# Kernel optimization log

Measured on AMD Instinct MI355X. Metric: run time of the kernel, lower is better.

The kernel has to match this reference:

```python
import jax, jax.numpy as jnp
import numpy as np

K = 8
W_CONST = 0.01
EPS = 1e-8


def _normalize(v, eps=1e-8):
    return v / (jnp.linalg.norm(v, axis=-1, keepdims=True) + eps)


def _coarse_normal(x, vertices, vertex_normals):
    # x: (N,3); vertices, vertex_normals: (V,3)
    # brute-force KNN (ascending by squared distance, like cKDTree.query)
    d2_all = jnp.sum((x[:, None, :] - vertices[None, :, :]) ** 2, axis=-1)  # (N,V)
    neg_d2, idx = jax.lax.top_k(-d2_all, K)  # sorted ascending distance
    d2 = -neg_d2                                                    # (N,K)
    v_knn = vertices[idx]                                           # (N,K,3)
    n_knn = vertex_normals[idx]                                     # (N,K,3)
    d2c = jnp.maximum(d2, EPS)
    inv_d2 = 1.0 / d2c                                              # (N,K)
    term_knn = jnp.sum(n_knn * inv_d2[..., None], axis=1)           # (N,3)
    v1 = v_knn[:, 0]                                                # nearest vertex
    d2_v1 = jnp.maximum(jnp.sum((x - v1) ** 2, axis=-1), EPS)       # (N,)
    term_dir = (x - v1) / (W_CONST * d2_v1[:, None])
    W = jnp.sum(inv_d2, axis=1) + 1.0 / W_CONST                     # (N,)
    n_tilde = (term_knn + term_dir) / W[:, None]
    nc = _normalize(n_tilde)
    return nc, v1


def _ray_mesh_first_hit(origins, dirs, tri0, e1, e2):
    # Moller-Trumbore, all points vs all faces. origins/dirs: (N,3); tri0/e1/e2: (F,3)
    pvec = jnp.cross(dirs[:, None, :], e2[None, :, :])              # (N,F,3)
    det = jnp.einsum('fk,nfk->nf', e1, pvec)                        # (N,F)
    ok_det = jnp.abs(det) > EPS
    inv_det = jnp.where(ok_det, 1.0 / jnp.where(ok_det, det, 1.0), 0.0)
    tvec = origins[:, None, :] - tri0[None, :, :]                   # (N,F,3)
    u = jnp.sum(tvec * pvec, axis=-1) * inv_det
    qvec = jnp.cross(tvec, e1[None, :, :])                          # (N,F,3)
    v = jnp.einsum('nk,nfk->nf', dirs, qvec) * inv_det
    t = jnp.einsum('fk,nfk->nf', e2, qvec) * inv_det
    valid = ok_det & (u >= 0.0) & (v >= 0.0) & (u + v <= 1.0) & (t > EPS)
    t_masked = jnp.where(valid, t, jnp.inf)
    t_min = jnp.min(t_masked, axis=1)                               # first hit along ray
    hit = jnp.isfinite(t_min)
    loc = origins + dirs * jnp.where(hit, t_min, 0.0)[:, None]
    return hit, loc


def _project(x, vertices, vertex_normals, faces):
    nc, v1 = _coarse_normal(x, vertices, vertex_normals)
    tri0 = vertices[faces[:, 0]]
    e1 = vertices[faces[:, 1]] - tri0
    e2 = vertices[faces[:, 2]] - tri0
    # primary cast along -nc
    hit1, loc1 = _ray_mesh_first_hit(x, -nc, tri0, e1, e2)
    # fallback cast toward nearest vertex
    dir_fb = _normalize(v1 - x)
    hit2, loc2 = _ray_mesh_first_hit(x, dir_fb, tri0, e1, e2)
    xc = jnp.where(hit1[:, None], loc1, jnp.where(hit2[:, None], loc2, v1))
    s = jnp.sum((x - xc) * nc, axis=-1, keepdims=True)              # (N,1)
    return xc, s, nc


def setup_inputs() -> dict:
    key = jax.random.key(0)
    k1, k2, k3, k4 = jax.random.split(key, 4)
    N, V, F = 2048, 8192, 8192
    x = jax.random.normal(k1, (N, 3), dtype=jnp.float32)
    vertices = jax.random.normal(k2, (V, 3), dtype=jnp.float32)
    vertex_normals = _normalize(jax.random.normal(k3, (V, 3), dtype=jnp.float32))
    faces = jax.random.randint(k4, (F, 3), 0, V, dtype=jnp.int32)
    return {"x": x, "vertices": vertices, "vertex_normals": vertex_normals, "faces": faces}


def reference(x, vertices, vertex_normals, faces):
    # returns (xc:(N,3), s:(N,1), nc:(N,3)) like ProjectionFn.forward
    return _project(x, vertices, vertex_normals, faces)
```

## Files before the change

### kernel.cpp

```cpp
#include <hip/hip_runtime.h>
#include <math.h>

#pragma float_control(precise, on)

#define EPSF 1e-8f


__global__ void __launch_bounds__(512) knn_prep_kernel(
    const float* __restrict__ x, const float* __restrict__ verts,
    const float* __restrict__ vnorm, const int* __restrict__ faces,
    float* __restrict__ tri, float* __restrict__ ncw,
    float* __restrict__ v1w, float* __restrict__ dfbw,
    int N, int V, int F) {
#pragma clang fp contract(off)
    int b = blockIdx.x;
    int tid = threadIdx.x;
    int wave = tid >> 6;
    int lane = tid & 63;
    int pA = 2 * b;
    if (pA >= N) return;
    int pB = pA + 1;
    bool hasB = pB < N;
    int pBs = hasB ? pB : pA;

    for (int gt = b * 512 + tid; gt < F; gt += gridDim.x * 512) {
        int f0 = faces[gt * 3 + 0];
        int f1 = faces[gt * 3 + 1];
        int f2 = faces[gt * 3 + 2];
        float t0x = verts[f0 * 3 + 0], t0y = verts[f0 * 3 + 1], t0z = verts[f0 * 3 + 2];
        float ax = verts[f1 * 3 + 0], ay = verts[f1 * 3 + 1], az = verts[f1 * 3 + 2];
        float bx = verts[f2 * 3 + 0], by = verts[f2 * 3 + 1], bz = verts[f2 * 3 + 2];
        float4* t4 = (float4*)(tri + (size_t)gt * 12);
        t4[0] = make_float4(t0x, t0y, t0z, ax - t0x);
        t4[1] = make_float4(ay - t0y, az - t0z, bx - t0x, by - t0y);
        t4[2] = make_float4(bz - t0z, 0.f, 0.f, 0.f);
    }

    float axx = x[pA * 3 + 0], axy = x[pA * 3 + 1], axz = x[pA * 3 + 2];
    float bxx = x[pBs * 3 + 0], bxy = x[pBs * 3 + 1], bxz = x[pBs * 3 + 2];

    unsigned long long la[8], lb[8];
#pragma unroll
    for (int i = 0; i < 8; ++i) { la[i] = ~0ULL; lb[i] = ~0ULL; }

    for (int v = tid; v < V; v += 512) {
        float vx = verts[v * 3 + 0];
        float vy = verts[v * 3 + 1];
        float vz = verts[v * 3 + 2];

        float dxa = axx - vx, dya = axy - vy, dza = axz - vz;
        float d2a = ((dxa * dxa) + (dya * dya)) + (dza * dza);
        unsigned long long kA =
            (((unsigned long long)__float_as_uint(d2a)) << 32) | (unsigned int)v;
        if (kA < la[7]) {
            la[7] = kA;
#pragma unroll
            for (int j = 7; j > 0; --j) {
                if (la[j] < la[j - 1]) {
                    unsigned long long t = la[j];
                    la[j] = la[j - 1];
                    la[j - 1] = t;
                }
            }
        }

        float dxb = bxx - vx, dyb = bxy - vy, dzb = bxz - vz;
        float d2b = ((dxb * dxb) + (dyb * dyb)) + (dzb * dzb);
        unsigned long long kB =
            (((unsigned long long)__float_as_uint(d2b)) << 32) | (unsigned int)v;
        if (kB < lb[7]) {
            lb[7] = kB;
#pragma unroll
            for (int j = 7; j > 0; --j) {
                if (lb[j] < lb[j - 1]) {
                    unsigned long long t = lb[j];
                    lb[j] = lb[j - 1];
                    lb[j - 1] = t;
                }
            }
        }
    }

    __shared__ unsigned long long candA[64], candB[64];
#pragma unroll
    for (int j = 0; j < 8; ++j) {
        unsigned long long mA = la[0];
        unsigned long long mB = lb[0];
#pragma unroll
        for (int s = 1; s < 64; s <<= 1) {
            unsigned long long oA = __shfl_xor(mA, s, 64);
            if (oA < mA) mA = oA;
            unsigned long long oB = __shfl_xor(mB, s, 64);
            if (oB < mB) mB = oB;
        }
        if (la[0] == mA) {
#pragma unroll
            for (int t = 0; t < 7; ++t) la[t] = la[t + 1];
            la[7] = ~0ULL;
        }
        if (lb[0] == mB) {
#pragma unroll
            for (int t = 0; t < 7; ++t) lb[t] = lb[t + 1];
            lb[7] = ~0ULL;
        }
        if (lane == 0) { candA[wave * 8 + j] = mA; candB[wave * 8 + j] = mB; }
    }
    __syncthreads();

    if (wave > 1) return;
    if (wave == 1 && !hasB) return;

    unsigned long long c0 = (wave == 0) ? candA[lane] : candB[lane];
    unsigned long long sel[8];
#pragma unroll
    for (int j = 0; j < 8; ++j) {
        unsigned long long m = c0;
#pragma unroll
        for (int s = 1; s < 64; s <<= 1) {
            unsigned long long o = __shfl_xor(m, s, 64);
            if (o < m) m = o;
        }
        if (c0 == m) c0 = ~0ULL;
        sel[j] = m;
    }

    if (lane != 0) return;
    int p = (wave == 0) ? pA : pB;
    float xx = (wave == 0) ? axx : bxx;
    float xy = (wave == 0) ? axy : bxy;
    float xz = (wave == 0) ? axz : bxz;

    float invk[8];
    float nsx = 0.f, nsy = 0.f, nsz = 0.f;
#pragma unroll
    for (int j = 0; j < 8; ++j) {
        int id = (int)(sel[j] & 0xffffffffu);
        float d2 = __uint_as_float((unsigned int)(sel[j] >> 32));
        float inv = 1.0f / fmaxf(d2, EPSF);
        invk[j] = inv;
        nsx = nsx + vnorm[id * 3 + 0] * inv;
        nsy = nsy + vnorm[id * 3 + 1] * inv;
        nsz = nsz + vnorm[id * 3 + 2] * inv;
    }
    float Wsum = ((invk[0] + invk[1]) + (invk[2] + invk[3])) +
                 ((invk[4] + invk[5]) + (invk[6] + invk[7]));

    int id0 = (int)(sel[0] & 0xffffffffu);
    float v1x = verts[id0 * 3 + 0];
    float v1y = verts[id0 * 3 + 1];
    float v1z = verts[id0 * 3 + 2];

    float dxv = xx - v1x, dyv = xy - v1y, dzv = xz - v1z;
    float d2v1 = fmaxf(((dxv * dxv) + (dyv * dyv)) + (dzv * dzv), EPSF);
    float den = 0.01f * d2v1;
    float tdx = dxv / den, tdy = dyv / den, tdz = dzv / den;

    float W = Wsum + 100.0f;
    float ntx = (nsx + tdx) / W;
    float nty = (nsy + tdy) / W;
    float ntz = (nsz + tdz) / W;
    float nrm = sqrtf(((ntx * ntx) + (nty * nty)) + (ntz * ntz)) + 1e-8f;
    float ncx = ntx / nrm, ncy = nty / nrm, ncz = ntz / nrm;

    float fx = v1x - xx, fy = v1y - xy, fz = v1z - xz;
    float fn = sqrtf(((fx * fx) + (fy * fy)) + (fz * fz)) + 1e-8f;
    fx = fx / fn; fy = fy / fn; fz = fz / fn;

    ncw[p * 3 + 0] = ncx; ncw[p * 3 + 1] = ncy; ncw[p * 3 + 2] = ncz;
    v1w[p * 3 + 0] = v1x; v1w[p * 3 + 1] = v1y; v1w[p * 3 + 2] = v1z;
    dfbw[p * 3 + 0] = fx; dfbw[p * 3 + 1] = fy; dfbw[p * 3 + 2] = fz;
}

__device__ __forceinline__ float mt_test(
    float ox, float oy, float oz, float dx, float dy, float dz,
    const float4 A, const float4 B, const float4 C, float tb) {
#pragma clang fp contract(off)
    const float M = 1e-5f;
    float e1x = A.w, e1y = B.x, e1z = B.y;
    float e2x = B.z, e2y = B.w, e2z = C.x;
    float tvx = ox - A.x;
    float tvy = oy - A.y;
    float tvz = oz - A.z;
    float qx = (tvy * e1z) - (tvz * e1y);
    float qy = (tvz * e1x) - (tvx * e1z);
    float qz = (tvx * e1y) - (tvy * e1x);
    float tq = ((e2x * qx) + (e2y * qy)) + (e2z * qz);
    float px = (dy * e2z) - (dz * e2y);
    float py = (dz * e2x) - (dx * e2z);
    float pz = (dx * e2y) - (dy * e2x);
    float det = ((e1x * px) + (e1y * py)) + (e1z * pz);
    bool ok = fabsf(det) > EPSF;
    float inv = ok ? (1.0f / det) : 0.0f;
    float u = (((tvx * px) + (tvy * py)) + (tvz * pz)) * inv;
    float v = (((dx * qx) + (dy * qy)) + (dz * qz)) * inv;
    float t = tq * inv;
    bool valid = ok && (u >= -M) && (v >= -M) && ((u + v) <= 1.0f + M) && (t > EPSF);
    return (valid && t < tb) ? t : tb;
}

__global__ void __launch_bounds__(512) ray_fin_kernel(
    const float* __restrict__ x, const float* __restrict__ tri,
    const float* __restrict__ ncw, const float* __restrict__ v1w,
    const float* __restrict__ dfbw, float* __restrict__ out, int N, int F) {
#pragma clang fp contract(off)
    __shared__ unsigned int redA[8], redB[8];
    __shared__ unsigned int u1As, u1Bs, u2As, u2Bs, hAf, hBf;
    int b = blockIdx.x;
    int tid = threadIdx.x;
    int wave = tid >> 6;
    int lane = tid & 63;
    int pA = 2 * b;
    if (pA >= N) return;
    int pB = pA + 1;
    bool hasB = pB < N;
    int pBs = hasB ? pB : pA;

    float axx = x[pA * 3 + 0], axy = x[pA * 3 + 1], axz = x[pA * 3 + 2];
    float Ancx = ncw[pA * 3 + 0], Ancy = ncw[pA * 3 + 1], Ancz = ncw[pA * 3 + 2];
    float Adbx = dfbw[pA * 3 + 0], Adby = dfbw[pA * 3 + 1], Adbz = dfbw[pA * 3 + 2];
    float Adax = -Ancx, Aday = -Ancy, Adaz = -Ancz;

    float bxx = x[pBs * 3 + 0], bxy = x[pBs * 3 + 1], bxz = x[pBs * 3 + 2];
    float Bncx = ncw[pBs * 3 + 0], Bncy = ncw[pBs * 3 + 1], Bncz = ncw[pBs * 3 + 2];
    float Bdbx = dfbw[pBs * 3 + 0], Bdby = dfbw[pBs * 3 + 1], Bdbz = dfbw[pBs * 3 + 2];
    float Bdax = -Bncx, Bday = -Bncy, Bdaz = -Bncz;

    const float INF = __uint_as_float(0x7f800000u);

    float tA = INF, tB = INF;
    for (int fi = tid; fi < F; fi += 512) {
        const float4 A4 = *(const float4*)(tri + (size_t)fi * 12);
        const float4 B4 = *(const float4*)(tri + (size_t)fi * 12 + 4);
        const float4 C4 = *(const float4*)(tri + (size_t)fi * 12 + 8);
        tA = mt_test(axx, axy, axz, Adax, Aday, Adaz, A4, B4, C4, tA);
        tB = mt_test(bxx, bxy, bxz, Bdax, Bday, Bdaz, A4, B4, C4, tB);
    }

    {
        unsigned int ma = __float_as_uint(tA);
        unsigned int mb = __float_as_uint(tB);
#pragma unroll
        for (int s = 1; s < 64; s <<= 1) {
            unsigned int oa = __shfl_xor(ma, s, 64);
            if (oa < ma) ma = oa;
            unsigned int ob = __shfl_xor(mb, s, 64);
            if (ob < mb) mb = ob;
        }
        if (lane == 0) { redA[wave] = ma; redB[wave] = mb; }
    }
    __syncthreads();
    if (tid == 0) {
        unsigned int u1A = min(min(min(redA[0], redA[1]), min(redA[2], redA[3])),
                               min(min(redA[4], redA[5]), min(redA[6], redA[7])));
        unsigned int u1B = min(min(min(redB[0], redB[1]), min(redB[2], redB[3])),
                               min(min(redB[4], redB[5]), min(redB[6], redB[7])));
        u1As = u1A; u1Bs = u1B;
        hAf = (u1A < 0x7f800000u) ? 1u : 0u;
        hBf = (u1B < 0x7f800000u) ? 1u : 0u;
    }
    __syncthreads();

    bool needA = (hAf == 0u);
    bool needB = hasB && (hBf == 0u);
    if (needA || needB) {
        float sA = INF, sB = INF;
        for (int fi = tid; fi < F; fi += 512) {
            const float4 A4 = *(const float4*)(tri + (size_t)fi * 12);
            const float4 B4 = *(const float4*)(tri + (size_t)fi * 12 + 4);
            const float4 C4 = *(const float4*)(tri + (size_t)fi * 12 + 8);
            if (needA) sA = mt_test(axx, axy, axz, Adbx, Adby, Adbz, A4, B4, C4, sA);
            if (needB) sB = mt_test(bxx, bxy, bxz, Bdbx, Bdby, Bdbz, A4, B4, C4, sB);
        }
        unsigned int ma = __float_as_uint(sA);
        unsigned int mb = __float_as_uint(sB);
#pragma unroll
        for (int s = 1; s < 64; s <<= 1) {
            unsigned int oa = __shfl_xor(ma, s, 64);
            if (oa < ma) ma = oa;
            unsigned int ob = __shfl_xor(mb, s, 64);
            if (ob < mb) mb = ob;
        }
        if (lane == 0) { redA[wave] = ma; redB[wave] = mb; }
        __syncthreads();
        if (tid == 0) {
            u2As = min(min(min(redA[0], redA[1]), min(redA[2], redA[3])),
                       min(min(redA[4], redA[5]), min(redA[6], redA[7])));
            u2Bs = min(min(min(redB[0], redB[1]), min(redB[2], redB[3])),
                       min(min(redB[4], redB[5]), min(redB[6], redB[7])));
        }
    }

    if (tid != 0) return;
    {
        float t1 = __uint_as_float(u1As);
        bool h1 = t1 < INF;
        float t2 = h1 ? INF : __uint_as_float(u2As);
        bool h2 = t2 < INF;
        float xcx, xcy, xcz;
        if (h1) {
            xcx = axx + ((-Ancx) * t1);
            xcy = axy + ((-Ancy) * t1);
            xcz = axz + ((-Ancz) * t1);
        } else if (h2) {
            xcx = axx + (Adbx * t2);
            xcy = axy + (Adby * t2);
            xcz = axz + (Adbz * t2);
        } else {
            xcx = v1w[pA * 3 + 0]; xcy = v1w[pA * 3 + 1]; xcz = v1w[pA * 3 + 2];
        }
        float s = (((axx - xcx) * Ancx) + ((axy - xcy) * Ancy)) + ((axz - xcz) * Ancz);
        out[pA * 3 + 0] = xcx;
        out[pA * 3 + 1] = xcy;
        out[pA * 3 + 2] = xcz;
        out[3 * N + pA] = s;
        out[4 * N + pA * 3 + 0] = Ancx;
        out[4 * N + pA * 3 + 1] = Ancy;
        out[4 * N + pA * 3 + 2] = Ancz;
    }
    if (hasB) {
        float t1 = __uint_as_float(u1Bs);
        bool h1 = t1 < INF;
        float t2 = h1 ? INF : __uint_as_float(u2Bs);
        bool h2 = t2 < INF;
        float xcx, xcy, xcz;
        if (h1) {
            xcx = bxx + ((-Bncx) * t1);
            xcy = bxy + ((-Bncy) * t1);
            xcz = bxz + ((-Bncz) * t1);
        } else if (h2) {
            xcx = bxx + (Bdbx * t2);
            xcy = bxy + (Bdby * t2);
            xcz = bxz + (Bdbz * t2);
        } else {
            xcx = v1w[pB * 3 + 0]; xcy = v1w[pB * 3 + 1]; xcz = v1w[pB * 3 + 2];
        }
        float s = (((bxx - xcx) * Bncx) + ((bxy - xcy) * Bncy)) + ((bxz - xcz) * Bncz);
        out[pB * 3 + 0] = xcx;
        out[pB * 3 + 1] = xcy;
        out[pB * 3 + 2] = xcz;
        out[3 * N + pB] = s;
        out[4 * N + pB * 3 + 0] = Bncx;
        out[4 * N + pB * 3 + 1] = Bncy;
        out[4 * N + pB * 3 + 2] = Bncz;
    }
}

extern "C" void kernel_launch(void* const* d_in, const int* in_sizes, int n_in,
                              void* d_out, int out_size, void* d_ws, size_t ws_size,
                              hipStream_t stream) {
    const float* x     = (const float*)d_in[0];
    const float* verts = (const float*)d_in[1];
    const float* vnorm = (const float*)d_in[2];
    const int*   faces = (const int*)d_in[3];
    int N = in_sizes[0] / 3;
    int V = in_sizes[1] / 3;
    int F = in_sizes[3] / 3;

    float* tri  = (float*)d_ws;
    float* ncw  = tri + (size_t)F * 12;
    float* v1w  = ncw + 3 * N;
    float* dfbw = v1w + 3 * N;

    int pblocks = (N + 1) / 2;
    hipLaunchKernelGGL(knn_prep_kernel, dim3(pblocks), dim3(512), 0, stream,
                       x, verts, vnorm, faces, tri, ncw, v1w, dfbw, N, V, F);
    hipLaunchKernelGGL(ray_fin_kernel, dim3(pblocks), dim3(512), 0, stream,
                       x, tri, ncw, v1w, dfbw, (float*)d_out, N, F);
}
```

Before: 135.6 us.

## Fuse KNN normal estimation into ray-casting kernel; split triangle prep out

Moves the per-point KNN and coarse-normal computation into the same block that performs the ray-triangle tests, passing the normal, nearest vertex and fallback direction through shared memory instead of global workspace. Triangle edge precomputation becomes its own small kernel. This removes the global round-trip of per-point intermediates and lets the KNN phase of one block overlap with the ray phase of others. In exchange, the fused kernel uses more registers and shared memory, which may lower occupancy.

```diff
diff --git a/kernel.cpp b/kernel.cpp
--- a/kernel.cpp
+++ b/kernel.cpp
@@ -6,169 +6,22 @@
 #define EPSF 1e-8f
 
 
-__global__ void __launch_bounds__(512) knn_prep_kernel(
-    const float* __restrict__ x, const float* __restrict__ verts,
-    const float* __restrict__ vnorm, const int* __restrict__ faces,
-    float* __restrict__ tri, float* __restrict__ ncw,
-    float* __restrict__ v1w, float* __restrict__ dfbw,
-    int N, int V, int F) {
+__global__ void __launch_bounds__(512) tri_prep_kernel(
+    const float* __restrict__ verts, const int* __restrict__ faces,
+    float* __restrict__ tri, int F) {
 #pragma clang fp contract(off)
-    int b = blockIdx.x;
-    int tid = threadIdx.x;
-    int wave = tid >> 6;
-    int lane = tid & 63;
-    int pA = 2 * b;
-    if (pA >= N) return;
-    int pB = pA + 1;
-    bool hasB = pB < N;
-    int pBs = hasB ? pB : pA;
-
-    for (int gt = b * 512 + tid; gt < F; gt += gridDim.x * 512) {
-        int f0 = faces[gt * 3 + 0];
-        int f1 = faces[gt * 3 + 1];
-        int f2 = faces[gt * 3 + 2];
-        float t0x = verts[f0 * 3 + 0], t0y = verts[f0 * 3 + 1], t0z = verts[f0 * 3 + 2];
-        float ax = verts[f1 * 3 + 0], ay = verts[f1 * 3 + 1], az = verts[f1 * 3 + 2];
-        float bx = verts[f2 * 3 + 0], by = verts[f2 * 3 + 1], bz = verts[f2 * 3 + 2];
-        float4* t4 = (float4*)(tri + (size_t)gt * 12);
-        t4[0] = make_float4(t0x, t0y, t0z, ax - t0x);
-        t4[1] = make_float4(ay - t0y, az - t0z, bx - t0x, by - t0y);
-        t4[2] = make_float4(bz - t0z, 0.f, 0.f, 0.f);
-    }
-
-    float axx = x[pA * 3 + 0], axy = x[pA * 3 + 1], axz = x[pA * 3 + 2];
-    float bxx = x[pBs * 3 + 0], bxy = x[pBs * 3 + 1], bxz = x[pBs * 3 + 2];
-
-    unsigned long long la[8], lb[8];
-#pragma unroll
-    for (int i = 0; i < 8; ++i) { la[i] = ~0ULL; lb[i] = ~0ULL; }
-
-    for (int v = tid; v < V; v += 512) {
-        float vx = verts[v * 3 + 0];
-        float vy = verts[v * 3 + 1];
-        float vz = verts[v * 3 + 2];
-
-        float dxa = axx - vx, dya = axy - vy, dza = axz - vz;
-        float d2a = ((dxa * dxa) + (dya * dya)) + (dza * dza);
-        unsigned long long kA =
-            (((unsigned long long)__float_as_uint(d2a)) << 32) | (unsigned int)v;
-        if (kA < la[7]) {
-            la[7] = kA;
-#pragma unroll
-            for (int j = 7; j > 0; --j) {
-                if (la[j] < la[j - 1]) {
-                    unsigned long long t = la[j];
-                    la[j] = la[j - 1];
-                    la[j - 1] = t;
-                }
-            }
-        }
-
-        float dxb = bxx - vx, dyb = bxy - vy, dzb = bxz - vz;
-        float d2b = ((dxb * dxb) + (dyb * dyb)) + (dzb * dzb);
-        unsigned long long kB =
-            (((unsigned long long)__float_as_uint(d2b)) << 32) | (unsigned int)v;
-        if (kB < lb[7]) {
-            lb[7] = kB;
-#pragma unroll
-            for (int j = 7; j > 0; --j) {
-                if (lb[j] < lb[j - 1]) {
-                    unsigned long long t = lb[j];
-                    lb[j] = lb[j - 1];
-                    lb[j - 1] = t;
-                }
-            }
-        }
-    }
-
-    __shared__ unsigned long long candA[64], candB[64];
-#pragma unroll
-    for (int j = 0; j < 8; ++j) {
-        unsigned long long mA = la[0];
-        unsigned long long mB = lb[0];
-#pragma unroll
-        for (int s = 1; s < 64; s <<= 1) {
-            unsigned long long oA = __shfl_xor(mA, s, 64);
-            if (oA < mA) mA = oA;
-            unsigned long long oB = __shfl_xor(mB, s, 64);
-            if (oB < mB) mB = oB;
-        }
-        if (la[0] == mA) {
-#pragma unroll
-            for (int t = 0; t < 7; ++t) la[t] = la[t + 1];
-            la[7] = ~0ULL;
-        }
-        if (lb[0] == mB) {
-#pragma unroll
-            for (int t = 0; t < 7; ++t) lb[t] = lb[t + 1];
-            lb[7] = ~0ULL;
-        }
-        if (lane == 0) { candA[wave * 8 + j] = mA; candB[wave * 8 + j] = mB; }
-    }
-    __syncthreads();
-
-    if (wave > 1) return;
-    if (wave == 1 && !hasB) return;
-
-    unsigned long long c0 = (wave == 0) ? candA[lane] : candB[lane];
-    unsigned long long sel[8];
-#pragma unroll
-    for (int j = 0; j < 8; ++j) {
-        unsigned long long m = c0;
-#pragma unroll
-        for (int s = 1; s < 64; s <<= 1) {
-            unsigned long long o = __shfl_xor(m, s, 64);
-            if (o < m) m = o;
-        }
-        if (c0 == m) c0 = ~0ULL;
-        sel[j] = m;
-    }
-
-    if (lane != 0) return;
-    int p = (wave == 0) ? pA : pB;
-    float xx = (wave == 0) ? axx : bxx;
-    float xy = (wave == 0) ? axy : bxy;
-    float xz = (wave == 0) ? axz : bxz;
-
-    float invk[8];
-    float nsx = 0.f, nsy = 0.f, nsz = 0.f;
-#pragma unroll
-    for (int j = 0; j < 8; ++j) {
-        int id = (int)(sel[j] & 0xffffffffu);
-        float d2 = __uint_as_float((unsigned int)(sel[j] >> 32));
-        float inv = 1.0f / fmaxf(d2, EPSF);
-        invk[j] = inv;
-        nsx = nsx + vnorm[id * 3 + 0] * inv;
-        nsy = nsy + vnorm[id * 3 + 1] * inv;
-        nsz = nsz + vnorm[id * 3 + 2] * inv;
-    }
-    float Wsum = ((invk[0] + invk[1]) + (invk[2] + invk[3])) +
-                 ((invk[4] + invk[5]) + (invk[6] + invk[7]));
-
-    int id0 = (int)(sel[0] & 0xffffffffu);
-    float v1x = verts[id0 * 3 + 0];
-    float v1y = verts[id0 * 3 + 1];
-    float v1z = verts[id0 * 3 + 2];
-
-    float dxv = xx - v1x, dyv = xy - v1y, dzv = xz - v1z;
-    float d2v1 = fmaxf(((dxv * dxv) + (dyv * dyv)) + (dzv * dzv), EPSF);
-    float den = 0.01f * d2v1;
-    float tdx = dxv / den, tdy = dyv / den, tdz = dzv / den;
-
-    float W = Wsum + 100.0f;
-    float ntx = (nsx + tdx) / W;
-    float nty = (nsy + tdy) / W;
-    float ntz = (nsz + tdz) / W;
-    float nrm = sqrtf(((ntx * ntx) + (nty * nty)) + (ntz * ntz)) + 1e-8f;
-    float ncx = ntx / nrm, ncy = nty / nrm, ncz = ntz / nrm;
-
-    float fx = v1x - xx, fy = v1y - xy, fz = v1z - xz;
-    float fn = sqrtf(((fx * fx) + (fy * fy)) + (fz * fz)) + 1e-8f;
-    fx = fx / fn; fy = fy / fn; fz = fz / fn;
-
-    ncw[p * 3 + 0] = ncx; ncw[p * 3 + 1] = ncy; ncw[p * 3 + 2] = ncz;
-    v1w[p * 3 + 0] = v1x; v1w[p * 3 + 1] = v1y; v1w[p * 3 + 2] = v1z;
-    dfbw[p * 3 + 0] = fx; dfbw[p * 3 + 1] = fy; dfbw[p * 3 + 2] = fz;
+    int gt = blockIdx.x * 512 + threadIdx.x;
+    if (gt >= F) return;
+    int f0 = faces[gt * 3 + 0];
+    int f1 = faces[gt * 3 + 1];
+    int f2 = faces[gt * 3 + 2];
+    float t0x = verts[f0 * 3 + 0], t0y = verts[f0 * 3 + 1], t0z = verts[f0 * 3 + 2];
+    float ax = verts[f1 * 3 + 0], ay = verts[f1 * 3 + 1], az = verts[f1 * 3 + 2];
+    float bx = verts[f2 * 3 + 0], by = verts[f2 * 3 + 1], bz = verts[f2 * 3 + 2];
+    float4* t4 = (float4*)(tri + (size_t)gt * 12);
+    t4[0] = make_float4(t0x, t0y, t0z, ax - t0x);
+    t4[1] = make_float4(ay - t0y, az - t0z, bx - t0x, by - t0y);
+    t4[2] = make_float4(bz - t0z, 0.f, 0.f, 0.f);
 }
 
 __device__ __forceinline__ float mt_test(
@@ -198,13 +51,16 @@
     return (valid && t < tb) ? t : tb;
 }
 
-__global__ void __launch_bounds__(512) ray_fin_kernel(
-    const float* __restrict__ x, const float* __restrict__ tri,
-    const float* __restrict__ ncw, const float* __restrict__ v1w,
-    const float* __restrict__ dfbw, float* __restrict__ out, int N, int F) {
+__global__ void __launch_bounds__(512) fused_kernel(
+    const float* __restrict__ x, const float* __restrict__ verts,
+    const float* __restrict__ vnorm, const float* __restrict__ tri,
+    float* __restrict__ out, int N, int V, int F) {
 #pragma clang fp contract(off)
+    __shared__ unsigned long long candA[64], candB[64];
+    __shared__ float bcA[9], bcB[9];
     __shared__ unsigned int redA[8], redB[8];
     __shared__ unsigned int u1As, u1Bs, u2As, u2Bs, hAf, hBf;
+
     int b = blockIdx.x;
     int tid = threadIdx.x;
     int wave = tid >> 6;
@@ -216,13 +72,142 @@
     int pBs = hasB ? pB : pA;
 
     float axx = x[pA * 3 + 0], axy = x[pA * 3 + 1], axz = x[pA * 3 + 2];
-    float Ancx = ncw[pA * 3 + 0], Ancy = ncw[pA * 3 + 1], Ancz = ncw[pA * 3 + 2];
-    float Adbx = dfbw[pA * 3 + 0], Adby = dfbw[pA * 3 + 1], Adbz = dfbw[pA * 3 + 2];
+    float bxx = x[pBs * 3 + 0], bxy = x[pBs * 3 + 1], bxz = x[pBs * 3 + 2];
+
+    unsigned long long la[8], lb[8];
+#pragma unroll
+    for (int i = 0; i < 8; ++i) { la[i] = ~0ULL; lb[i] = ~0ULL; }
+
+    for (int v = tid; v < V; v += 512) {
+        float vx = verts[v * 3 + 0];
+        float vy = verts[v * 3 + 1];
+        float vz = verts[v * 3 + 2];
+
+        float dxa = axx - vx, dya = axy - vy, dza = axz - vz;
+        float d2a = ((dxa * dxa) + (dya * dya)) + (dza * dza);
+        unsigned long long kA =
+            (((unsigned long long)__float_as_uint(d2a)) << 32) | (unsigned int)v;
+        if (kA < la[7]) {
+            la[7] = kA;
+#pragma unroll
+            for (int j = 7; j > 0; --j) {
+                if (la[j] < la[j - 1]) {
+                    unsigned long long t = la[j];
+                    la[j] = la[j - 1];
+                    la[j - 1] = t;
+                }
+            }
+        }
+
+        float dxb = bxx - vx, dyb = bxy - vy, dzb = bxz - vz;
+        float d2b = ((dxb * dxb) + (dyb * dyb)) + (dzb * dzb);
+        unsigned long long kB =
+            (((unsigned long long)__float_as_uint(d2b)) << 32) | (unsigned int)v;
+        if (kB < lb[7]) {
+            lb[7] = kB;
+#pragma unroll
+            for (int j = 7; j > 0; --j) {
+                if (lb[j] < lb[j - 1]) {
+                    unsigned long long t = lb[j];
+                    lb[j] = lb[j - 1];
+                    lb[j - 1] = t;
+                }
+            }
+        }
+    }
+
+#pragma unroll
+    for (int j = 0; j < 8; ++j) {
+        unsigned long long mA = la[0];
+        unsigned long long mB = lb[0];
+#pragma unroll
+        for (int s = 1; s < 64; s <<= 1) {
+            unsigned long long oA = __shfl_xor(mA, s, 64);
+            if (oA < mA) mA = oA;
+            unsigned long long oB = __shfl_xor(mB, s, 64);
+            if (oB < mB) mB = oB;
+        }
+        if (la[0] == mA) {
+#pragma unroll
+            for (int t = 0; t < 7; ++t) la[t] = la[t + 1];
+            la[7] = ~0ULL;
+        }
+        if (lb[0] == mB) {
+#pragma unroll
+            for (int t = 0; t < 7; ++t) lb[t] = lb[t + 1];
+            lb[7] = ~0ULL;
+        }
+        if (lane == 0) { candA[wave * 8 + j] = mA; candB[wave * 8 + j] = mB; }
+    }
+    __syncthreads();
+
+    if (wave < 2) {
+        unsigned long long c0 = (wave == 0) ? candA[lane] : candB[lane];
+        unsigned long long sel[8];
+#pragma unroll
+        for (int j = 0; j < 8; ++j) {
+            unsigned long long m = c0;
+#pragma unroll
+            for (int s = 1; s < 64; s <<= 1) {
+                unsigned long long o = __shfl_xor(m, s, 64);
+                if (o < m) m = o;
+            }
+            if (c0 == m) c0 = ~0ULL;
+            sel[j] = m;
+        }
+
+        if (lane == 0) {
+            float xx = (wave == 0) ? axx : bxx;
+            float xy = (wave == 0) ? axy : bxy;
+            float xz = (wave == 0) ? axz : bxz;
+
+            float invk[8];
+            float nsx = 0.f, nsy = 0.f, nsz = 0.f;
+#pragma unroll
+            for (int j = 0; j < 8; ++j) {
+                int id = (int)(sel[j] & 0xffffffffu);
+                float d2 = __uint_as_float((unsigned int)(sel[j] >> 32));
+                float inv = 1.0f / fmaxf(d2, EPSF);
+                invk[j] = inv;
+                nsx = nsx + vnorm[id * 3 + 0] * inv;
+                nsy = nsy + vnorm[id * 3 + 1] * inv;
+                nsz = nsz + vnorm[id * 3 + 2] * inv;
+            }
+            float Wsum = ((invk[0] + invk[1]) + (invk[2] + invk[3])) +
+                         ((invk[4] + invk[5]) + (invk[6] + invk[7]));
+
+            int id0 = (int)(sel[0] & 0xffffffffu);
+            float v1x = verts[id0 * 3 + 0];
+            float v1y = verts[id0 * 3 + 1];
+            float v1z = verts[id0 * 3 + 2];
+
+            float dxv = xx - v1x, dyv = xy - v1y, dzv = xz - v1z;
+            float d2v1 = fmaxf(((dxv * dxv) + (dyv * dyv)) + (dzv * dzv), EPSF);
+            float den = 0.01f * d2v1;
+            float tdx = dxv / den, tdy = dyv / den, tdz = dzv / den;
+
+            float W = Wsum + 100.0f;
+            float ntx = (nsx + tdx) / W;
+            float nty = (nsy + tdy) / W;
+            float ntz = (nsz + tdz) / W;
+            float nrm = sqrtf(((ntx * ntx) + (nty * nty)) + (ntz * ntz)) + 1e-8f;
+
+            float fx = v1x - xx, fy = v1y - xy, fz = v1z - xz;
+            float fn = sqrtf(((fx * fx) + (fy * fy)) + (fz * fz)) + 1e-8f;
+
+            float* bc = (wave == 0) ? bcA : bcB;
+            bc[0] = ntx / nrm; bc[1] = nty / nrm; bc[2] = ntz / nrm;
+            bc[3] = v1x; bc[4] = v1y; bc[5] = v1z;
+            bc[6] = fx / fn; bc[7] = fy / fn; bc[8] = fz / fn;
+        }
+    }
+    __syncthreads();
+
+    float Ancx = bcA[0], Ancy = bcA[1], Ancz = bcA[2];
+    float Adbx = bcA[6], Adby = bcA[7], Adbz = bcA[8];
     float Adax = -Ancx, Aday = -Ancy, Adaz = -Ancz;
-
-    float bxx = x[pBs * 3 + 0], bxy = x[pBs * 3 + 1], bxz = x[pBs * 3 + 2];
-    float Bncx = ncw[pBs * 3 + 0], Bncy = ncw[pBs * 3 + 1], Bncz = ncw[pBs * 3 + 2];
-    float Bdbx = dfbw[pBs * 3 + 0], Bdby = dfbw[pBs * 3 + 1], Bdbz = dfbw[pBs * 3 + 2];
+    float Bncx = bcB[0], Bncy = bcB[1], Bncz = bcB[2];
+    float Bdbx = bcB[6], Bdby = bcB[7], Bdbz = bcB[8];
     float Bdax = -Bncx, Bday = -Bncy, Bdaz = -Bncz;
 
     const float INF = __uint_as_float(0x7f800000u);
@@ -306,7 +291,7 @@
             xcy = axy + (Adby * t2);
             xcz = axz + (Adbz * t2);
         } else {
-            xcx = v1w[pA * 3 + 0]; xcy = v1w[pA * 3 + 1]; xcz = v1w[pA * 3 + 2];
+            xcx = bcA[3]; xcy = bcA[4]; xcz = bcA[5];
         }
         float s = (((axx - xcx) * Ancx) + ((axy - xcy) * Ancy)) + ((axz - xcz) * Ancz);
         out[pA * 3 + 0] = xcx;
@@ -332,16 +317,16 @@
             xcy = bxy + (Bdby * t2);
             xcz = bxz + (Bdbz * t2);
         } else {
-            xcx = v1w[pB * 3 + 0]; xcy = v1w[pB * 3 + 1]; xcz = v1w[pB * 3 + 2];
+            xcx = bcB[3]; xcy = bcB[4]; xcz = bcB[5];
         }
         float s = (((bxx - xcx) * Bncx) + ((bxy - xcy) * Bncy)) + ((bxz - xcz) * Bncz);
         out[pB * 3 + 0] = xcx;
         out[pB * 3 + 1] = xcy;
         out[pB * 3 + 2] = xcz;
-        out[3 * N + pB] = s;
         out[4 * N + pB * 3 + 0] = Bncx;
         out[4 * N + pB * 3 + 1] = Bncy;
         out[4 * N + pB * 3 + 2] = Bncz;
+        out[3 * N + pB] = s;
     }
 }
 
@@ -356,14 +341,12 @@
     int V = in_sizes[1] / 3;
     int F = in_sizes[3] / 3;
 
-    float* tri  = (float*)d_ws;
-    float* ncw  = tri + (size_t)F * 12;
-    float* v1w  = ncw + 3 * N;
-    float* dfbw = v1w + 3 * N;
-
+    float* tri = (float*)d_ws;
+
+    int tblocks = (F + 511) / 512;
+    hipLaunchKernelGGL(tri_prep_kernel, dim3(tblocks), dim3(512), 0, stream,
+                       verts, faces, tri, F);
     int pblocks = (N + 1) / 2;
-    hipLaunchKernelGGL(knn_prep_kernel, dim3(pblocks), dim3(512), 0, stream,
-                       x, verts, vnorm, faces, tri, ncw, v1w, dfbw, N, V, F);
-    hipLaunchKernelGGL(ray_fin_kernel, dim3(pblocks), dim3(512), 0, stream,
-                       x, tri, ncw, v1w, dfbw, (float*)d_out, N, F);
+    hipLaunchKernelGGL(fused_kernel, dim3(pblocks), dim3(512), 0, stream,
+                       x, verts, vnorm, tri, (float*)d_out, N, V, F);
 }
```

After: 133.0 us. No clear change (-1.9%).
